# Kernel optimization log

Measured on AMD Instinct MI355X. Metric: run time of the kernel, lower is better.

## Reference

```python
import jax, jax.numpy as jnp
import numpy as np

NC = 6            # CPAB tessellation cells (tess_size=6, zero_boundary=True)
DIM = NC - 1      # theta dimension = 5
SIG_LEN = 2048
CHANNELS = 3
BATCH = 256
FC_IN = 64 * 168  # flattened net_part1 output for signal_len=2048
NUM_SCALING = 0   # N in transform_data_ss
EPS_BN = 1e-5


def _cpab_basis():
    """QR null-space basis of the CPAB continuity + zero-boundary constraints.
    Params ordered [a_1,b_1,...,a_NC,b_NC]; v(x)=a_c x + b_c on cell c."""
    nc = NC
    L = np.zeros((nc + 1, 2 * nc))
    for k in range(1, nc):  # continuity at internal knots x_k = k/nc
        xk = k / nc
        L[k - 1, 2 * (k - 1)] = xk
        L[k - 1, 2 * (k - 1) + 1] = 1.0
        L[k - 1, 2 * k] = -xk
        L[k - 1, 2 * k + 1] = -1.0
    L[nc - 1, 1] = 1.0        # v(0) = 0  -> b_1 = 0
    L[nc, 2 * (nc - 1)] = 1.0  # v(1) = 0 -> a_nc + b_nc = 0
    L[nc, 2 * nc - 1] = 1.0
    Q, _ = np.linalg.qr(L.T, mode='complete')
    return np.ascontiguousarray(Q[:, nc + 1:]).astype(np.float32)  # (12, 5)


def _conv1d(x, w, b):
    y = jax.lax.conv_general_dilated(x, w, (1,), 'VALID',
                                     dimension_numbers=('NCH', 'OIH', 'NCH'))
    return y + b[None, :, None]


def _maxpool1d(x, k, s):
    return jax.lax.reduce_window(x, -jnp.inf, jax.lax.max, (1, 1, k), (1, 1, s), 'VALID')


def _bn(x, g, b, m, v):  # eval-mode BatchNorm1d
    return (x - m[None, :, None]) * (g / jnp.sqrt(v + EPS_BN))[None, :, None] + b[None, :, None]


def _integrate(x, A):
    """Exact CPAB 1D flow integration over t=1 with cell-crossing handling.
    x: (B, n) points in [0,1]; A: (B, NC, 2) per-cell (a, b). Monotone
    trajectories cross at most NC-1 boundaries -> fixed NC+1 iterations."""
    a_all, b_all = A[:, :, 0], A[:, :, 1]
    t = jnp.ones_like(x)
    for _ in range(NC + 1):
        c = jnp.clip(jnp.floor(x * NC).astype(jnp.int32), 0, NC - 1)
        a = jnp.take_along_axis(a_all, c, axis=1)
        b = jnp.take_along_axis(b_all, c, axis=1)
        v = a * x + b
        xb = jnp.where(v >= 0, (c + 1).astype(x.dtype) / NC, c.astype(x.dtype) / NC)
        big_a = jnp.abs(a) > 1e-8
        a_s = jnp.where(big_a, a, 1.0)
        z = x + b / a_s        # shifted coord: x(t) = z*exp(a t) - b/a
        zb = xb + b / a_s
        ratio = zb / jnp.where(jnp.abs(z) > 1e-12, z, 1e-12)
        t_exp = jnp.log(jnp.maximum(ratio, 1e-12)) / a_s
        v_s = jnp.where(jnp.abs(v) > 1e-12, v, 1.0)
        t_lin = (xb - x) / v_s
        thit = jnp.where(big_a, t_exp, t_lin)
        valid = (jnp.abs(v) > 1e-12) & (thit > 0) & (jnp.where(big_a, ratio, 1.0) > 0)
        thit = jnp.where(valid, thit, jnp.inf)
        tau = jnp.minimum(t, thit)
        x_new = jnp.where(big_a, z * jnp.exp(a * tau) - (z - x), x + b * tau)
        hit = thit <= t
        nudge = jnp.where(v >= 0, 1e-6, -1e-6)  # push into next cell
        x = jnp.clip(jnp.where(hit, xb + nudge, x_new), 0.0, 1.0)
        t = jnp.maximum(t - tau, 0.0)
    return x


def _interp1d(data, pos):
    """data: (B, L, C); pos: (B, n) in [0,1] -> (B, n, C) linear interpolation."""
    Lw = data.shape[1]
    p = jnp.clip(pos, 0.0, 1.0) * (Lw - 1)
    x0 = jnp.clip(jnp.floor(p).astype(jnp.int32), 0, Lw - 2)
    w = (p - x0.astype(p.dtype))[:, :, None]
    d0 = jnp.take_along_axis(data, x0[:, :, None], axis=1)
    d1 = jnp.take_along_axis(data, (x0 + 1)[:, :, None], axis=1)
    return d0 * (1.0 - w) + d1 * w


def _transform_data_ss(data, theta, basis, outsize, N):
    """CPAB scaling-and-squaring warp of data (B, L, C) by theta (B, DIM)."""
    Bsz = theta.shape[0]
    A = (theta @ basis.T).reshape(Bsz, NC, 2) / (2.0 ** N)
    grid = jnp.linspace(0.0, 1.0, outsize, dtype=data.dtype)
    grid_t = _integrate(jnp.broadcast_to(grid, (Bsz, outsize)), A)
    for _ in range(N):  # squaring: compose the warp with itself
        grid_t = _interp1d(grid_t[:, :, None], grid_t)[:, :, 0]
    return _interp1d(data, grid_t)


def reference(x, conv1_w, conv1_b, bn1_g, bn1_b, bn1_m, bn1_v,
              conv2_w, conv2_b, bn2_g, bn2_b, bn2_m, bn2_v,
              conv3_w, conv3_b, bn3_g, bn3_b, bn3_m, bn3_v,
              fc1_w, fc1_b, fc2_w, fc2_b, fc3_w, fc3_b, fc4_w, fc4_b, basis):
    # localization net (n_recurrence = 1, back_version = True)
    h = jax.nn.relu(_maxpool1d(_bn(_conv1d(x, conv1_w, conv1_b), bn1_g, bn1_b, bn1_m, bn1_v), 3, 2))
    h = jax.nn.relu(_maxpool1d(_bn(_conv1d(h, conv2_w, conv2_b), bn2_g, bn2_b, bn2_m, bn2_v), 3, 3))
    h = jax.nn.relu(_maxpool1d(_bn(_conv1d(h, conv3_w, conv3_b), bn3_g, bn3_b, bn3_m, bn3_v), 3, 2))
    xs = h.reshape(h.shape[0], -1)  # (B, 64*168)
    xs = jax.nn.relu(xs @ fc1_w.T + fc1_b)
    xs = jax.nn.relu(xs @ fc2_w.T + fc2_b)
    xs = jax.nn.relu(xs @ fc3_w.T + fc3_b)
    theta = jnp.tanh(xs @ fc4_w.T + fc4_b)  # (B, 5)
    data = jnp.transpose(x, (0, 2, 1))       # (B, L, C)
    warped = _transform_data_ss(data, theta, basis, SIG_LEN, NUM_SCALING)
    return jnp.transpose(warped, (0, 2, 1))  # (B, C, L)


def setup_inputs() -> dict:
    key = jax.random.key(0)
    ks = jax.random.split(key, 16)
    def nrm(k, shape, scale):
        return (jax.random.normal(k, shape) * scale).astype(jnp.float32)
    inp = {}
    inp['x'] = jax.random.normal(ks[0], (BATCH, CHANNELS, SIG_LEN), dtype=jnp.float32)
    inp['conv1_w'] = nrm(ks[1], (128, CHANNELS, 3), (CHANNELS * 3) ** -0.5)
    inp['conv1_b'] = nrm(ks[2], (128,), 0.01)
    inp['bn1_g'] = jnp.ones((128,), jnp.float32)
    inp['bn1_b'] = jnp.zeros((128,), jnp.float32)
    inp['bn1_m'] = nrm(ks[3], (128,), 0.1)
    inp['bn1_v'] = jnp.ones((128,), jnp.float32)
    inp['conv2_w'] = nrm(ks[4], (64, 128, 5), (128 * 5) ** -0.5)
    inp['conv2_b'] = nrm(ks[5], (64,), 0.01)
    inp['bn2_g'] = jnp.ones((64,), jnp.float32)
    inp['bn2_b'] = jnp.zeros((64,), jnp.float32)
    inp['bn2_m'] = nrm(ks[6], (64,), 0.1)
    inp['bn2_v'] = jnp.ones((64,), jnp.float32)
    inp['conv3_w'] = nrm(ks[7], (64, 64, 3), (64 * 3) ** -0.5)
    inp['conv3_b'] = nrm(ks[8], (64,), 0.01)
    inp['bn3_g'] = jnp.ones((64,), jnp.float32)
    inp['bn3_b'] = jnp.zeros((64,), jnp.float32)
    inp['bn3_m'] = nrm(ks[9], (64,), 0.1)
    inp['bn3_v'] = jnp.ones((64,), jnp.float32)
    inp['fc1_w'] = nrm(ks[10], (48, FC_IN), FC_IN ** -0.5)
    inp['fc1_b'] = jnp.zeros((48,), jnp.float32)
    inp['fc2_w'] = nrm(ks[11], (32, 48), 48 ** -0.5)
    inp['fc2_b'] = jnp.zeros((32,), jnp.float32)
    inp['fc3_w'] = nrm(ks[12], (16, 32), 32 ** -0.5)
    inp['fc3_b'] = jnp.zeros((16,), jnp.float32)
    # near-identity warp head (original zero-inits weight, identity bias)
    inp['fc4_w'] = nrm(ks[13], (DIM, 16), 0.01)
    inp['fc4_b'] = nrm(ks[14], (DIM,), 0.01)
    inp['basis'] = jnp.asarray(_cpab_basis())
    return inp
```

## Files before the change

kernel.cpp:

```cpp
#include <hip/hip_runtime.h>
#include <math.h>

#define BATCH   256
#define SIGLEN  2048
#define L1OUT   1022
#define L2OUT   339
#define L3OUT   168
#define FCIN    10752

#define TP2   21
#define NROW  68
#define H1S   136

#define TU3   28

#define KC1   12
#define KCL   (FCIN/KC1)

typedef float f32x4  __attribute__((ext_vector_type(4)));
typedef float f32x16 __attribute__((ext_vector_type(16)));
typedef short s16x8  __attribute__((ext_vector_type(8)));

__device__ __forceinline__ unsigned short f2bf(float f) {
    unsigned int u = __float_as_uint(f);
    return (unsigned short)((u + 0x7fffu + ((u >> 16) & 1u)) >> 16);
}
__device__ __forceinline__ float bf2f(unsigned short h) {
    return __uint_as_float(((unsigned int)h) << 16);
}

__launch_bounds__(256)
__global__ void prep_kernel(
    const float* __restrict__ conv1_b,
    const float* __restrict__ g1, const float* __restrict__ b1,
    const float* __restrict__ m1, const float* __restrict__ v1,
    const float* __restrict__ conv2_w, const float* __restrict__ conv2_b,
    const float* __restrict__ g2, const float* __restrict__ b2,
    const float* __restrict__ m2, const float* __restrict__ v2,
    const float* __restrict__ conv3_w, const float* __restrict__ conv3_b,
    const float* __restrict__ g3, const float* __restrict__ b3,
    const float* __restrict__ m3, const float* __restrict__ v3,
    const float* __restrict__ fc1_w,
    unsigned short* __restrict__ w2hi, unsigned short* __restrict__ w2lo,
    unsigned short* __restrict__ w3hi, unsigned short* __restrict__ w3lo,
    float* __restrict__ wp1,
    float* __restrict__ so1, float* __restrict__ so2, float* __restrict__ so3)
{
    int tid = blockIdx.x * 256 + threadIdx.x;
    int stride = gridDim.x * 256;
    for (int i = tid; i < 64*128*5; i += stride) {
        int co = i / 640; int rr = i - co*640; int ci = rr / 5; int k = rr - ci*5;
        float w = conv2_w[i];
        unsigned short hi = f2bf(w);
        unsigned short lo = f2bf(w - bf2f(hi));
        int seg = k*8 + (ci >> 4);
        int dst = ((seg*2 + (co >> 5))*32 + (co & 31))*16 + (ci & 15);
        w2hi[dst] = hi;
        w2lo[dst] = lo;
    }
    for (int i = tid; i < 64*64*3; i += stride) {
        int co = i / 192; int r = i - co*192; int ci = r / 3; int k = r - ci*3;
        float w = conv3_w[i];
        unsigned short hi = f2bf(w);
        unsigned short lo = f2bf(w - bf2f(hi));
        int dst = ((k*2 + (ci >> 5))*64 + co)*32 + (ci & 31);
        w3hi[dst] = hi;
        w3lo[dst] = lo;
    }
    for (int i = tid; i < 48*FCIN; i += stride) {
        int o = i / FCIN; int r = i - o*FCIN;
        int co = r / L3OUT, u = r - co*L3OUT;
        wp1[o*FCIN + u*64 + co] = fc1_w[i];
    }
    if (tid < 128) {
        float s = g1[tid] / sqrtf(v1[tid] + 1e-5f);
        so1[tid]       = s;
        so1[128 + tid] = (conv1_b[tid] - m1[tid]) * s + b1[tid];
    }
    if (tid < 64) {
        float s2 = g2[tid] / sqrtf(v2[tid] + 1e-5f);
        so2[tid]      = s2;
        so2[64 + tid] = (conv2_b[tid] - m2[tid]) * s2 + b2[tid];
        float s3 = g3[tid] / sqrtf(v3[tid] + 1e-5f);
        so3[tid]      = s3;
        so3[64 + tid] = (conv3_b[tid] - m3[tid]) * s3 + b3[tid];
    }
}

__launch_bounds__(256, 4)
__global__ void conv12_kernel(
    const float* __restrict__ x, const float* __restrict__ w1,
    const unsigned short* __restrict__ w2hi, const unsigned short* __restrict__ w2lo,
    const float* __restrict__ so1, const float* __restrict__ so2,
    unsigned int* __restrict__ h2p)
{
    __shared__ unsigned short h1hi[NROW * H1S];
    __shared__ unsigned short h1lo[NROW * H1S];

    int t  = threadIdx.x;
    int b  = blockIdx.x;
    int u0 = blockIdx.y * TP2;
    int q0 = 3 * u0;
    int wv = __builtin_amdgcn_readfirstlane(t >> 6);
    int l  = t & 63;

    float wr[2][9];
    float s1r[2], o1r[2];
    #pragma unroll
    for (int h = 0; h < 2; ++h) {
        int ch = l + 64*h;
        #pragma unroll
        for (int j = 0; j < 9; ++j) wr[h][j] = w1[ch*9 + j];
        s1r[h] = so1[ch]; o1r[h] = so1[128 + ch];
    }
    for (int s = 0; s < 17; ++s) {
        int r = 4*s + wv;
        int xbase = 2*(q0 + r);
        float xv[3][5];
        #pragma unroll
        for (int ci = 0; ci < 3; ++ci) {
            const float* xp = x + (b*3 + ci)*SIGLEN;
            #pragma unroll
            for (int d = 0; d < 5; ++d) {
                int xi = xbase + d; xi = xi < SIGLEN ? xi : SIGLEN - 1;
                xv[ci][d] = xp[xi];
            }
        }
        #pragma unroll
        for (int h = 0; h < 2; ++h) {
            float r0 = 0.f, r1 = 0.f, r2 = 0.f;
            #pragma unroll
            for (int ci = 0; ci < 3; ++ci) {
                float wA = wr[h][ci*3], wB = wr[h][ci*3+1], wC = wr[h][ci*3+2];
                r0 = fmaf(xv[ci][0], wA, fmaf(xv[ci][1], wB, fmaf(xv[ci][2], wC, r0)));
                r1 = fmaf(xv[ci][1], wA, fmaf(xv[ci][2], wB, fmaf(xv[ci][3], wC, r1)));
                r2 = fmaf(xv[ci][2], wA, fmaf(xv[ci][3], wB, fmaf(xv[ci][4], wC, r2)));
            }
            float mx = fmaxf(r0, fmaxf(r1, r2));
            float v  = fmaxf(fmaf(s1r[h], mx, o1r[h]), 0.f);
            unsigned short hi = f2bf(v);
            unsigned short lo = f2bf(v - bf2f(hi));
            h1hi[r*H1S + l + 64*h] = hi;
            h1lo[r*H1S + l + 64*h] = lo;
        }
    }
    __syncthreads();

    int ph  = wv >> 1;
    int chf = wv & 1;
    int r32 = l & 31;
    int oct = l >> 5;

    f32x16 acc = (f32x16)(0.f);
    const unsigned short* whB = w2hi + (chf*32 + r32)*16 + oct*8;
    const unsigned short* wlB = w2lo + (chf*32 + r32)*16 + oct*8;

    for (int ks = 0; ks < 5; ++ks) {
        #pragma unroll
        for (int cb = 0; cb < 8; ++cb) {
            int seg = ks*8 + cb;
            s16x8 wh = *(const s16x8*)(whB + seg*1024);
            s16x8 wl = *(const s16x8*)(wlB + seg*1024);
            int row = ph*32 + r32 + ks;
            s16x8 ah = *(const s16x8*)&h1hi[row*H1S + cb*16 + oct*8];
            s16x8 al = *(const s16x8*)&h1lo[row*H1S + cb*16 + oct*8];
            acc = __builtin_amdgcn_mfma_f32_32x32x16_bf16(ah, wh, acc, 0, 0, 0);
            acc = __builtin_amdgcn_mfma_f32_32x32x16_bf16(al, wh, acc, 0, 0, 0);
            acc = __builtin_amdgcn_mfma_f32_32x32x16_bf16(ah, wl, acc, 0, 0, 0);
        }
    }
    __syncthreads();

    float* c2 = (float*)h1hi;
    #pragma unroll
    for (int rg = 0; rg < 16; ++rg) {
        int row = (rg & 3) + 8*(rg >> 2) + 4*oct;
        c2[(ph*32 + row)*65 + chf*32 + r32] = acc[rg];
    }
    __syncthreads();

    #pragma unroll
    for (int it = 0; it < 6; ++it) {
        int idx = t + it*256;
        if (idx < TP2*64) {
            int ul = idx >> 6, co = idx & 63;
            int u = u0 + ul;
            if (u < L2OUT) {
                float v0 = c2[(3*ul  )*65 + co];
                float v1 = c2[(3*ul+1)*65 + co];
                float v2 = c2[(3*ul+2)*65 + co];
                float mm = fmaxf(v0, fmaxf(v1, v2));
                float v  = fmaxf(fmaf(so2[co], mm, so2[64 + co]), 0.f);
                unsigned short hi = f2bf(v);
                unsigned short lo = f2bf(v - bf2f(hi));
                h2p[(b*L2OUT + u)*64 + co] = (unsigned int)hi | ((unsigned int)lo << 16);
            }
        }
    }
}

__launch_bounds__(256, 4)
__global__ void conv3_kernel(
    const unsigned int* __restrict__ h2p,
    const unsigned short* __restrict__ w3hi, const unsigned short* __restrict__ w3lo,
    const float* __restrict__ so3, float* __restrict__ xs)
{
    __shared__ unsigned short h3hi[66 * 72];
    __shared__ unsigned short h3lo[66 * 72];

    int t  = threadIdx.x;
    int b  = blockIdx.x;
    int u0 = blockIdx.y * TU3;
    int wv = __builtin_amdgcn_readfirstlane(t >> 6);
    int l  = t & 63;
    int m  = l & 15;
    int qd = l >> 4;

    for (int i = t; i < 66*64; i += 256) {
        int r = i >> 6, ci = i & 63;
        int g = 2*u0 + r; g = g > (L2OUT-1) ? (L2OUT-1) : g;
        unsigned int v = h2p[(b*L2OUT + g)*64 + ci];
        h3hi[r*72 + ci] = (unsigned short)(v & 0xffffu);
        h3lo[r*72 + ci] = (unsigned short)(v >> 16);
    }
    __syncthreads();

    s16x8 wh[6], wl[6];
    #pragma unroll
    for (int s = 0; s < 6; ++s) {
        wh[s] = *(const s16x8*)(w3hi + s*2048 + (wv*16 + m)*32 + qd*8);
        wl[s] = *(const s16x8*)(w3lo + s*2048 + (wv*16 + m)*32 + qd*8);
    }

    f32x4 acc[4] = {(f32x4)(0.f), (f32x4)(0.f), (f32x4)(0.f), (f32x4)(0.f)};
    #pragma unroll
    for (int pt = 0; pt < 4; ++pt) {
        #pragma unroll
        for (int s = 0; s < 6; ++s) {
            int row = pt*16 + m + (s >> 1);
            int off = (s & 1)*32 + qd*8;
            s16x8 ah = *(const s16x8*)&h3hi[row*72 + off];
            s16x8 al = *(const s16x8*)&h3lo[row*72 + off];
            acc[pt] = __builtin_amdgcn_mfma_f32_16x16x32_bf16(ah, wh[s], acc[pt], 0, 0, 0);
            acc[pt] = __builtin_amdgcn_mfma_f32_16x16x32_bf16(al, wh[s], acc[pt], 0, 0, 0);
            acc[pt] = __builtin_amdgcn_mfma_f32_16x16x32_bf16(ah, wl[s], acc[pt], 0, 0, 0);
        }
    }
    __syncthreads();

    float* c3 = (float*)h3hi;
    #pragma unroll
    for (int pt = 0; pt < 4; ++pt)
        #pragma unroll
        for (int rg = 0; rg < 4; ++rg)
            c3[(pt*16 + qd*4 + rg)*65 + wv*16 + m] = acc[pt][rg];
    __syncthreads();

    #pragma unroll
    for (int it = 0; it < 7; ++it) {
        int idx = t + it*256;
        if (idx < TU3*64) {
            int ul = idx >> 6, co = idx & 63;
            int p = 2*ul;
            float v0 = c3[(p  )*65 + co];
            float v1 = c3[(p+1)*65 + co];
            float v2 = c3[(p+2)*65 + co];
            float mm = fmaxf(v0, fmaxf(v1, v2));
            xs[b*FCIN + (u0 + ul)*64 + co] = fmaxf(fmaf(so3[co], mm, so3[64 + co]), 0.f);
        }
    }
}

__launch_bounds__(256)
__global__ void fc1_kernel(
    const float* __restrict__ xs, const float* __restrict__ w,
    float* __restrict__ part)
{
    int t = threadIdx.x, lane = t & 63, wid = t >> 6;
    int b0 = blockIdx.x * 4;
    int kc = blockIdx.y;
    int o0 = wid * 12;
    float acc[48];
    #pragma unroll
    for (int i = 0; i < 48; ++i) acc[i] = 0.f;

    int kbase = kc * KCL + lane;
    for (int ki = 0; ki < KCL/64; ++ki) {
        int k = kbase + ki * 64;
        float xv0 = xs[(b0 + 0) * FCIN + k];
        float xv1 = xs[(b0 + 1) * FCIN + k];
        float xv2 = xs[(b0 + 2) * FCIN + k];
        float xv3 = xs[(b0 + 3) * FCIN + k];
        #pragma unroll
        for (int j = 0; j < 12; ++j) {
            float ww = w[(o0 + j) * FCIN + k];
            acc[j]      += xv0 * ww;
            acc[12 + j] += xv1 * ww;
            acc[24 + j] += xv2 * ww;
            acc[36 + j] += xv3 * ww;
        }
    }
    #pragma unroll
    for (int i = 0; i < 48; ++i) {
        #pragma unroll
        for (int off = 32; off > 0; off >>= 1)
            acc[i] += __shfl_xor(acc[i], off, 64);
    }
    if (lane == 0) {
        #pragma unroll
        for (int bb = 0; bb < 4; ++bb)
            #pragma unroll
            for (int j = 0; j < 12; ++j)
                part[((b0 + bb) * 48 + o0 + j) * KC1 + kc] = acc[bb * 12 + j];
    }
}

__launch_bounds__(256)
__global__ void fc234_kernel(
    const float* __restrict__ part, const float* __restrict__ fc1_b,
    const float* __restrict__ fc2_w, const float* __restrict__ fc2_b,
    const float* __restrict__ fc3_w, const float* __restrict__ fc3_b,
    const float* __restrict__ fc4_w, const float* __restrict__ fc4_b,
    const float* __restrict__ basis, float* __restrict__ A)
{
    __shared__ float xsl[256 * 49];
    int t = threadIdx.x;
    for (int i = t; i < 256 * 48; i += 256) {
        const float4* p = (const float4*)&part[i * KC1];
        float4 pa = p[0], pb = p[1], pc = p[2];
        float sv = ((pa.x + pa.y) + (pa.z + pa.w))
                 + ((pb.x + pb.y) + (pb.z + pb.w))
                 + ((pc.x + pc.y) + (pc.z + pc.w));
        xsl[(i / 48) * 49 + (i % 48)] = fmaxf(sv + fc1_b[i % 48], 0.f);
    }
    __syncthreads();

    float xin[48];
    #pragma unroll
    for (int i = 0; i < 48; ++i) xin[i] = xsl[t * 49 + i];

    float h[32];
    for (int o = 0; o < 32; ++o) {
        float sv = fc2_b[o];
        #pragma unroll
        for (int i = 0; i < 48; ++i) sv = fmaf(fc2_w[o * 48 + i], xin[i], sv);
        h[o] = fmaxf(sv, 0.f);
    }
    float g[16];
    for (int o = 0; o < 16; ++o) {
        float sv = fc3_b[o];
        #pragma unroll
        for (int i = 0; i < 32; ++i) sv = fmaf(fc3_w[o * 32 + i], h[i], sv);
        g[o] = fmaxf(sv, 0.f);
    }
    float th[5];
    #pragma unroll
    for (int o = 0; o < 5; ++o) {
        float sv = fc4_b[o];
        #pragma unroll
        for (int i = 0; i < 16; ++i) sv = fmaf(fc4_w[o * 16 + i], g[i], sv);
        th[o] = tanhf(sv);
    }
    #pragma unroll
    for (int j = 0; j < 12; ++j) {
        float sv = 0.f;
        #pragma unroll
        for (int d = 0; d < 5; ++d) sv = fmaf(basis[j * 5 + d], th[d], sv);
        A[t * 12 + j] = sv;
    }
}

__launch_bounds__(256)
__global__ void warp_kernel(
    const float* __restrict__ x, const float* __restrict__ A,
    float* __restrict__ out)
{
    __shared__ float Al[12];
    int b = blockIdx.x;
    int i = blockIdx.y * 256 + threadIdx.x;
    if (threadIdx.x < 12) Al[threadIdx.x] = A[b * 12 + threadIdx.x];
    __syncthreads();

    float xp = (float)i / 2047.f;
    float t  = 1.f;
    for (int it = 0; it < 7; ++it) {
        int c = (int)floorf(xp * 6.f);
        c = min(max(c, 0), 5);
        float a  = Al[2 * c], bb = Al[2 * c + 1];
        float v  = a * xp + bb;
        float xb = (v >= 0.f) ? (float)(c + 1) / 6.f : (float)c / 6.f;
        bool  big_a = fabsf(a) > 1e-8f;
        float a_s = big_a ? a : 1.f;
        float z   = xp + bb / a_s;
        float zb  = xb + bb / a_s;
        float zden = (fabsf(z) > 1e-12f) ? z : 1e-12f;
        float ratio = zb / zden;
        float t_exp = logf(fmaxf(ratio, 1e-12f)) / a_s;
        float v_s   = (fabsf(v) > 1e-12f) ? v : 1.f;
        float t_lin = (xb - xp) / v_s;
        float thit  = big_a ? t_exp : t_lin;
        bool valid  = (fabsf(v) > 1e-12f) && (thit > 0.f) && ((big_a ? ratio : 1.f) > 0.f);
        if (!valid) thit = __builtin_inff();
        float tau   = fminf(t, thit);
        float x_new = big_a ? (z * expf(a * tau) - (z - xp)) : (xp + bb * tau);
        bool hit    = (thit <= t);
        float nudge = (v >= 0.f) ? 1e-6f : -1e-6f;
        xp = hit ? (xb + nudge) : x_new;
        xp = fminf(fmaxf(xp, 0.f), 1.f);
        t  = fmaxf(t - tau, 0.f);
    }
    float p = fminf(fmaxf(xp, 0.f), 1.f) * 2047.f;
    int i0 = (int)floorf(p);
    i0 = min(max(i0, 0), 2046);
    float w = p - (float)i0;
    #pragma unroll
    for (int c = 0; c < 3; ++c) {
        const float* d = &x[(b * 3 + c) * SIGLEN];
        out[(b * 3 + c) * SIGLEN + i] = d[i0] * (1.f - w) + d[i0 + 1] * w;
    }
}

extern "C" void kernel_launch(void* const* d_in, const int* in_sizes, int n_in,
                              void* d_out, int out_size, void* d_ws, size_t ws_size,
                              hipStream_t stream) {
    (void)in_sizes; (void)n_in; (void)out_size; (void)ws_size;
    const float* x       = (const float*)d_in[0];
    const float* conv1_w = (const float*)d_in[1];
    const float* conv1_b = (const float*)d_in[2];
    const float* bn1_g   = (const float*)d_in[3];
    const float* bn1_b   = (const float*)d_in[4];
    const float* bn1_m   = (const float*)d_in[5];
    const float* bn1_v   = (const float*)d_in[6];
    const float* conv2_w = (const float*)d_in[7];
    const float* conv2_b = (const float*)d_in[8];
    const float* bn2_g   = (const float*)d_in[9];
    const float* bn2_b   = (const float*)d_in[10];
    const float* bn2_m   = (const float*)d_in[11];
    const float* bn2_v   = (const float*)d_in[12];
    const float* conv3_w = (const float*)d_in[13];
    const float* conv3_b = (const float*)d_in[14];
    const float* bn3_g   = (const float*)d_in[15];
    const float* bn3_b   = (const float*)d_in[16];
    const float* bn3_m   = (const float*)d_in[17];
    const float* bn3_v   = (const float*)d_in[18];
    const float* fc1_w   = (const float*)d_in[19];
    const float* fc1_b   = (const float*)d_in[20];
    const float* fc2_w   = (const float*)d_in[21];
    const float* fc2_b   = (const float*)d_in[22];
    const float* fc3_w   = (const float*)d_in[23];
    const float* fc3_b   = (const float*)d_in[24];
    const float* fc4_w   = (const float*)d_in[25];
    const float* fc4_b   = (const float*)d_in[26];
    const float* basis   = (const float*)d_in[27];

    unsigned short* w2hi = (unsigned short*)d_ws;
    unsigned short* w2lo = w2hi + 40960;
    unsigned short* w3hi = w2lo + 40960;
    unsigned short* w3lo = w3hi + 12288;
    float* ws   = (float*)d_ws;
    float* so1  = ws + 53248;
    float* so2  = so1 + 256;
    float* so3  = so2 + 128;
    float* wp1  = so3 + 128;
    unsigned int* h2p = (unsigned int*)(wp1 + 516096);
    float* xs   = wp1 + 516096 + 5554176;
    float* part = xs  + 2752512;
    float* Aws  = part + 147456;

    prep_kernel<<<256, 256, 0, stream>>>(
        conv1_b, bn1_g, bn1_b, bn1_m, bn1_v,
        conv2_w, conv2_b, bn2_g, bn2_b, bn2_m, bn2_v,
        conv3_w, conv3_b, bn3_g, bn3_b, bn3_m, bn3_v,
        fc1_w, w2hi, w2lo, w3hi, w3lo, wp1, so1, so2, so3);

    dim3 g2(BATCH, (L2OUT + TP2 - 1) / TP2);
    conv12_kernel<<<g2, 256, 0, stream>>>(x, conv1_w, w2hi, w2lo, so1, so2, h2p);

    dim3 g3(BATCH, L3OUT / TU3);
    conv3_kernel<<<g3, 256, 0, stream>>>(h2p, w3hi, w3lo, so3, xs);

    dim3 gfc(BATCH / 4, KC1);
    fc1_kernel<<<gfc, 256, 0, stream>>>(xs, wp1, part);

    fc234_kernel<<<1, 256, 0, stream>>>(part, fc1_b, fc2_w, fc2_b, fc3_w, fc3_b,
                                        fc4_w, fc4_b, basis, Aws);

    dim3 g5(BATCH, SIGLEN / 256);
    warp_kernel<<<g5, 256, 0, stream>>>(x, Aws, (float*)d_out);
}
```

Before: 294.4 us.

## Fuse FC2-4 head into warp kernel, split conv2 MFMA K across waves, coalesce fc1 prep

```diff
diff --git a/kernel.cpp b/kernel.cpp
--- a/kernel.cpp
+++ b/kernel.cpp
@@ -69,8 +69,8 @@
     }
     for (int i = tid; i < 48*FCIN; i += stride) {
         int o = i / FCIN; int r = i - o*FCIN;
-        int co = r / L3OUT, u = r - co*L3OUT;
-        wp1[o*FCIN + u*64 + co] = fc1_w[i];
+        int u = r >> 6, co = r & 63;
+        wp1[i] = fc1_w[o*FCIN + co*L3OUT + u];
     }
     if (tid < 128) {
         float s = g1[tid] / sqrtf(v1[tid] + 1e-5f);
@@ -146,36 +146,54 @@
     }
     __syncthreads();
 
-    int ph  = wv >> 1;
     int chf = wv & 1;
+    int kh  = wv >> 1;
     int r32 = l & 31;
     int oct = l >> 5;
 
-    f32x16 acc = (f32x16)(0.f);
+    f32x16 acc0 = (f32x16)(0.f);
+    f32x16 acc1 = (f32x16)(0.f);
     const unsigned short* whB = w2hi + (chf*32 + r32)*16 + oct*8;
     const unsigned short* wlB = w2lo + (chf*32 + r32)*16 + oct*8;
 
-    for (int ks = 0; ks < 5; ++ks) {
-        #pragma unroll
-        for (int cb = 0; cb < 8; ++cb) {
-            int seg = ks*8 + cb;
-            s16x8 wh = *(const s16x8*)(whB + seg*1024);
-            s16x8 wl = *(const s16x8*)(wlB + seg*1024);
-            int row = ph*32 + r32 + ks;
-            s16x8 ah = *(const s16x8*)&h1hi[row*H1S + cb*16 + oct*8];
-            s16x8 al = *(const s16x8*)&h1lo[row*H1S + cb*16 + oct*8];
-            acc = __builtin_amdgcn_mfma_f32_32x32x16_bf16(ah, wh, acc, 0, 0, 0);
-            acc = __builtin_amdgcn_mfma_f32_32x32x16_bf16(al, wh, acc, 0, 0, 0);
-            acc = __builtin_amdgcn_mfma_f32_32x32x16_bf16(ah, wl, acc, 0, 0, 0);
-        }
+    #pragma unroll 4
+    for (int ss = 0; ss < 20; ++ss) {
+        int sg = kh*20 + ss;
+        int ks = sg >> 3, cb = sg & 7;
+        s16x8 wh = *(const s16x8*)(whB + sg*1024);
+        s16x8 wl = *(const s16x8*)(wlB + sg*1024);
+        int row0 = r32 + ks;
+        int row1 = 32 + r32 + ks;
+        s16x8 ah0 = *(const s16x8*)&h1hi[row0*H1S + cb*16 + oct*8];
+        s16x8 al0 = *(const s16x8*)&h1lo[row0*H1S + cb*16 + oct*8];
+        s16x8 ah1 = *(const s16x8*)&h1hi[row1*H1S + cb*16 + oct*8];
+        s16x8 al1 = *(const s16x8*)&h1lo[row1*H1S + cb*16 + oct*8];
+        acc0 = __builtin_amdgcn_mfma_f32_32x32x16_bf16(ah0, wh, acc0, 0, 0, 0);
+        acc1 = __builtin_amdgcn_mfma_f32_32x32x16_bf16(ah1, wh, acc1, 0, 0, 0);
+        acc0 = __builtin_amdgcn_mfma_f32_32x32x16_bf16(al0, wh, acc0, 0, 0, 0);
+        acc1 = __builtin_amdgcn_mfma_f32_32x32x16_bf16(al1, wh, acc1, 0, 0, 0);
+        acc0 = __builtin_amdgcn_mfma_f32_32x32x16_bf16(ah0, wl, acc0, 0, 0, 0);
+        acc1 = __builtin_amdgcn_mfma_f32_32x32x16_bf16(ah1, wl, acc1, 0, 0, 0);
     }
     __syncthreads();
 
     float* c2 = (float*)h1hi;
-    #pragma unroll
-    for (int rg = 0; rg < 16; ++rg) {
-        int row = (rg & 3) + 8*(rg >> 2) + 4*oct;
-        c2[(ph*32 + row)*65 + chf*32 + r32] = acc[rg];
+    if (kh == 0) {
+        #pragma unroll
+        for (int rg = 0; rg < 16; ++rg) {
+            int row = (rg & 3) + 8*(rg >> 2) + 4*oct;
+            c2[row*65        + chf*32 + r32] = acc0[rg];
+            c2[(32 + row)*65 + chf*32 + r32] = acc1[rg];
+        }
+    }
+    __syncthreads();
+    if (kh == 1) {
+        #pragma unroll
+        for (int rg = 0; rg < 16; ++rg) {
+            int row = (rg & 3) + 8*(rg >> 2) + 4*oct;
+            c2[row*65        + chf*32 + r32] += acc0[rg];
+            c2[(32 + row)*65 + chf*32 + r32] += acc1[rg];
+        }
     }
     __syncthreads();
 
@@ -316,73 +334,65 @@
 }
 
 __launch_bounds__(256)
-__global__ void fc234_kernel(
-    const float* __restrict__ part, const float* __restrict__ fc1_b,
+__global__ void warp_kernel(
+    const float* __restrict__ x, const float* __restrict__ part,
+    const float* __restrict__ fc1_b,
     const float* __restrict__ fc2_w, const float* __restrict__ fc2_b,
     const float* __restrict__ fc3_w, const float* __restrict__ fc3_b,
     const float* __restrict__ fc4_w, const float* __restrict__ fc4_b,
-    const float* __restrict__ basis, float* __restrict__ A)
+    const float* __restrict__ basis,
+    float* __restrict__ out)
 {
-    __shared__ float xsl[256 * 49];
+    __shared__ float xsl[48];
+    __shared__ float hl[32];
+    __shared__ float gl[16];
+    __shared__ float thl[5];
+    __shared__ float Al[12];
+
+    int b = blockIdx.x;
     int t = threadIdx.x;
-    for (int i = t; i < 256 * 48; i += 256) {
-        const float4* p = (const float4*)&part[i * KC1];
+    int i = blockIdx.y * 256 + t;
+
+    if (t < 48) {
+        const float4* p = (const float4*)&part[(b * 48 + t) * KC1];
         float4 pa = p[0], pb = p[1], pc = p[2];
         float sv = ((pa.x + pa.y) + (pa.z + pa.w))
                  + ((pb.x + pb.y) + (pb.z + pb.w))
                  + ((pc.x + pc.y) + (pc.z + pc.w));
-        xsl[(i / 48) * 49 + (i % 48)] = fmaxf(sv + fc1_b[i % 48], 0.f);
-    }
-    __syncthreads();
-
-    float xin[48];
-    #pragma unroll
-    for (int i = 0; i < 48; ++i) xin[i] = xsl[t * 49 + i];
-
-    float h[32];
-    for (int o = 0; o < 32; ++o) {
-        float sv = fc2_b[o];
-        #pragma unroll
-        for (int i = 0; i < 48; ++i) sv = fmaf(fc2_w[o * 48 + i], xin[i], sv);
-        h[o] = fmaxf(sv, 0.f);
-    }
-    float g[16];
-    for (int o = 0; o < 16; ++o) {
-        float sv = fc3_b[o];
-        #pragma unroll
-        for (int i = 0; i < 32; ++i) sv = fmaf(fc3_w[o * 32 + i], h[i], sv);
-        g[o] = fmaxf(sv, 0.f);
-    }
-    float th[5];
-    #pragma unroll
-    for (int o = 0; o < 5; ++o) {
-        float sv = fc4_b[o];
-        #pragma unroll
-        for (int i = 0; i < 16; ++i) sv = fmaf(fc4_w[o * 16 + i], g[i], sv);
-        th[o] = tanhf(sv);
-    }
-    #pragma unroll
-    for (int j = 0; j < 12; ++j) {
+        xsl[t] = fmaxf(sv + fc1_b[t], 0.f);
+    }
+    __syncthreads();
+    if (t < 32) {
+        float sv = fc2_b[t];
+        #pragma unroll
+        for (int k = 0; k < 48; ++k) sv = fmaf(fc2_w[t * 48 + k], xsl[k], sv);
+        hl[t] = fmaxf(sv, 0.f);
+    }
+    __syncthreads();
+    if (t < 16) {
+        float sv = fc3_b[t];
+        #pragma unroll
+        for (int k = 0; k < 32; ++k) sv = fmaf(fc3_w[t * 32 + k], hl[k], sv);
+        gl[t] = fmaxf(sv, 0.f);
+    }
+    __syncthreads();
+    if (t < 5) {
+        float sv = fc4_b[t];
+        #pragma unroll
+        for (int k = 0; k < 16; ++k) sv = fmaf(fc4_w[t * 16 + k], gl[k], sv);
+        thl[t] = tanhf(sv);
+    }
+    __syncthreads();
+    if (t < 12) {
         float sv = 0.f;
         #pragma unroll
-        for (int d = 0; d < 5; ++d) sv = fmaf(basis[j * 5 + d], th[d], sv);
-        A[t * 12 + j] = sv;
-    }
-}
-
-__launch_bounds__(256)
-__global__ void warp_kernel(
-    const float* __restrict__ x, const float* __restrict__ A,
-    float* __restrict__ out)
-{
-    __shared__ float Al[12];
-    int b = blockIdx.x;
-    int i = blockIdx.y * 256 + threadIdx.x;
-    if (threadIdx.x < 12) Al[threadIdx.x] = A[b * 12 + threadIdx.x];
+        for (int d = 0; d < 5; ++d) sv = fmaf(basis[t * 5 + d], thl[d], sv);
+        Al[t] = sv;
+    }
     __syncthreads();
 
     float xp = (float)i / 2047.f;
-    float t  = 1.f;
+    float tt = 1.f;
     for (int it = 0; it < 7; ++it) {
         int c = (int)floorf(xp * 6.f);
         c = min(max(c, 0), 5);
@@ -401,13 +411,13 @@
         float thit  = big_a ? t_exp : t_lin;
         bool valid  = (fabsf(v) > 1e-12f) && (thit > 0.f) && ((big_a ? ratio : 1.f) > 0.f);
         if (!valid) thit = __builtin_inff();
-        float tau   = fminf(t, thit);
+        float tau   = fminf(tt, thit);
         float x_new = big_a ? (z * expf(a * tau) - (z - xp)) : (xp + bb * tau);
-        bool hit    = (thit <= t);
+        bool hit    = (thit <= tt);
         float nudge = (v >= 0.f) ? 1e-6f : -1e-6f;
         xp = hit ? (xb + nudge) : x_new;
         xp = fminf(fmaxf(xp, 0.f), 1.f);
-        t  = fmaxf(t - tau, 0.f);
+        tt = fmaxf(tt - tau, 0.f);
     }
     float p = fminf(fmaxf(xp, 0.f), 1.f) * 2047.f;
     int i0 = (int)floorf(p);
@@ -465,7 +475,6 @@
     unsigned int* h2p = (unsigned int*)(wp1 + 516096);
     float* xs   = wp1 + 516096 + 5554176;
     float* part = xs  + 2752512;
-    float* Aws  = part + 147456;
 
     prep_kernel<<<256, 256, 0, stream>>>(
         conv1_b, bn1_g, bn1_b, bn1_m, bn1_v,
@@ -482,9 +491,8 @@
     dim3 gfc(BATCH / 4, KC1);
     fc1_kernel<<<gfc, 256, 0, stream>>>(xs, wp1, part);
 
-    fc234_kernel<<<1, 256, 0, stream>>>(part, fc1_b, fc2_w, fc2_b, fc3_w, fc3_b,
-                                        fc4_w, fc4_b, basis, Aws);
-
     dim3 g5(BATCH, SIGLEN / 256);
-    warp_kernel<<<g5, 256, 0, stream>>>(x, Aws, (float*)d_out);
-}
+    warp_kernel<<<g5, 256, 0, stream>>>(x, part, fc1_b, fc2_w, fc2_b,
+                                        fc3_w, fc3_b, fc4_w, fc4_b, basis,
+                                        (float*)d_out);
+}
```

Measured after the change: 262.2 us. 1.12x faster.
